# Kernel tuning notes

Hardware: AMD Instinct MI355X
Metric: run time of the kernel (lower is better)

## Reference

```python
import jax, jax.numpy as jnp
import numpy as np

TEMPERATURE = 1.0
EPS = 1e-12  # matches torch F.normalize default eps


def setup_inputs() -> dict:
    key = jax.random.key(0)
    k1, k2 = jax.random.split(key)
    B, N, D = 8, 2048, 768
    final_features = jax.random.normal(k1, (B, N, D), dtype=jnp.float32)
    mid_features = jax.random.normal(k2, (B, N, D), dtype=jnp.float32)
    return {"final_features": final_features, "mid_features": mid_features}


def reference(final_features, mid_features):
    B, N, D = final_features.shape
    dtype = final_features.dtype

    mid = mid_features.astype(jnp.float32)
    # L2-normalize along feature dim (torch F.normalize: x / max(||x||, eps))
    norm = jnp.maximum(jnp.linalg.norm(mid, axis=-1, keepdims=True), EPS)
    mid_n = mid / norm

    # [B, N, N] cosine similarity
    sim = jnp.einsum("bnd,bmd->bnm", mid_n, mid_n)
    # zero out diagonal (add_self_similarity=False): sim * (1 - eye)
    eye = jnp.eye(N, dtype=sim.dtype)
    sim = sim * (1.0 - eye)[None, :, :]

    # confidence = row-wise max of (zeroed-diagonal) similarity
    confidence = jnp.max(sim, axis=-1)  # [B, N]

    # softmax over scaled similarities (diagonal entries are exactly 0, kept in softmax)
    weights = jax.nn.softmax(sim / TEMPERATURE, axis=-1)  # [B, N, N]

    refined = jnp.einsum("bnm,bmd->bnd", weights, final_features.astype(jnp.float32))

    cw = confidence[..., None].astype(dtype)  # [B, N, 1]
    calibrated = cw * refined.astype(dtype) + (1.0 - cw) * final_features
    return calibrated
```

## Files before the change

### kernel.cpp

```cpp
#include <hip/hip_runtime.h>
#include <hip/hip_bf16.h>

static constexpr int BB = 8;
static constexpr int NN = 2048;
static constexpr int DD = 768;

typedef __attribute__((ext_vector_type(8))) __bf16 bf16x8;
typedef __attribute__((ext_vector_type(4))) float f32x4;

__device__ __forceinline__ void gload_lds16(const __hip_bfloat16* g, __hip_bfloat16* l) {
  __builtin_amdgcn_global_load_lds(
      (const __attribute__((address_space(1))) void*)g,
      (__attribute__((address_space(3))) void*)l,
      16, 0, 0);
}

__global__ void normalize_kernel(const float* __restrict__ mid, __hip_bfloat16* __restrict__ Qn,
                                 float* __restrict__ lsum, float* __restrict__ conf) {
  const int wave = threadIdx.x >> 6;
  const int lane = threadIdx.x & 63;
  const size_t row = (size_t)blockIdx.x * 4 + wave;
  if (lane == 0) { lsum[row] = 0.f; conf[row] = 0.f; }
  const float* src = mid + row * DD;

  float4 v[3];
  float ss = 0.f;
#pragma unroll
  for (int j = 0; j < 3; ++j) {
    v[j] = *(const float4*)(src + j * 256 + lane * 4);
    ss += v[j].x * v[j].x + v[j].y * v[j].y + v[j].z * v[j].z + v[j].w * v[j].w;
  }
#pragma unroll
  for (int o = 32; o; o >>= 1) ss += __shfl_xor(ss, o, 64);
  const float inv = 1.0f / fmaxf(sqrtf(ss), 1e-12f);

  __hip_bfloat16* dst = Qn + row * DD;
#pragma unroll
  for (int j = 0; j < 3; ++j) {
    union { ushort4 u; __hip_bfloat16 h[4]; } pk;
    pk.h[0] = __float2bfloat16(v[j].x * inv);
    pk.h[1] = __float2bfloat16(v[j].y * inv);
    pk.h[2] = __float2bfloat16(v[j].z * inv);
    pk.h[3] = __float2bfloat16(v[j].w * inv);
    *(ushort4*)(dst + j * 256 + lane * 4) = pk.u;
  }
}

__global__ void transpose_kernel(const float* __restrict__ F, __hip_bfloat16* __restrict__ Vt) {
  __shared__ __hip_bfloat16 tile[32][33];
  const int b = blockIdx.z;
  const int n0 = blockIdx.y * 32;
  const int d0 = blockIdx.x * 32;
  const int tx = threadIdx.x, ty = threadIdx.y;
#pragma unroll
  for (int i = 0; i < 4; ++i) {
    const int n = n0 + ty + i * 8;
    tile[ty + i * 8][tx] = __float2bfloat16(F[((size_t)b * NN + n) * DD + d0 + tx]);
  }
  __syncthreads();
#pragma unroll
  for (int i = 0; i < 4; ++i) {
    const int d = d0 + ty + i * 8;
    Vt[((size_t)b * DD + d) * NN + n0 + tx] = tile[tx][ty + i * 8];
  }
}

static constexpr int PTL = 136;
__global__ __launch_bounds__(256) void gemm_qk_kernel(
    const __hip_bfloat16* __restrict__ Qn,
    __hip_bfloat16* __restrict__ P,
    float* __restrict__ lsum,
    unsigned* __restrict__ conf) {
  __shared__ __hip_bfloat16 smem[4 * 128 * 64];

  const int d = blockIdx.x;
  const int b = d & 7;
  int rem = d >> 3;
  int ti = 0;
  while (rem >= 16 - ti) { rem -= 16 - ti; ++ti; }
  const int tj = ti + rem;
  const int rowBase = ti * 128;
  const int colBase = tj * 128;
  const bool offdiag = (ti != tj);

  const int t = threadIdx.x;
  const int lane = t & 63;
  const int wave = t >> 6;
  const int wRow = wave >> 1;
  const int wCol = wave & 1;
  const int quad = lane >> 4;
  const int l16 = lane & 15;

  const __hip_bfloat16* Abase = Qn + ((size_t)b * NN + rowBase) * DD;
  const __hip_bfloat16* Bbase = Qn + ((size_t)b * NN + colBase) * DD;

  int srow[4], scol[4], sc8[4];
#pragma unroll
  for (int i = 0; i < 4; ++i) {
    const int c = i * 256 + t;
    srow[i] = c >> 3;
    const int col8 = (c & 7) ^ ((c >> 3) & 7);
    scol[i] = col8 * 8;
    sc8[i] = c * 8;
  }

  f32x4 acc[4][4];
#pragma unroll
  for (int i = 0; i < 4; ++i)
#pragma unroll
    for (int j = 0; j < 4; ++j) acc[i][j] = (f32x4){0.f, 0.f, 0.f, 0.f};

  {
    __hip_bfloat16* As = smem;
    __hip_bfloat16* Bs = smem + 128 * 64;
#pragma unroll
    for (int i = 0; i < 4; ++i) {
      gload_lds16(Abase + (size_t)srow[i] * DD + scol[i], As + sc8[i]);
      gload_lds16(Bbase + (size_t)srow[i] * DD + scol[i], Bs + sc8[i]);
    }
  }

  constexpr int NK = DD / 64;
  for (int kk = 0; kk < NK; ++kk) {
    const int cur = kk & 1;
    __syncthreads();
    if (kk + 1 < NK) {
      __hip_bfloat16* As = smem + (1 - cur) * 2 * 128 * 64;
      __hip_bfloat16* Bs = As + 128 * 64;
      const int k0 = (kk + 1) * 64;
#pragma unroll
      for (int i = 0; i < 4; ++i) {
        gload_lds16(Abase + (size_t)srow[i] * DD + (k0 + scol[i]), As + sc8[i]);
        gload_lds16(Bbase + (size_t)srow[i] * DD + (k0 + scol[i]), Bs + sc8[i]);
      }
    }
    const __hip_bfloat16* As = smem + cur * 2 * 128 * 64;
    const __hip_bfloat16* Bs = As + 128 * 64;
#pragma unroll
    for (int ks = 0; ks < 2; ++ks) {
      bf16x8 af[4], bfr[4];
#pragma unroll
      for (int i = 0; i < 4; ++i) {
        const int rA = wRow * 64 + i * 16 + l16;
        const int rB = wCol * 64 + i * 16 + l16;
        const int pA = (ks * 4 + quad) ^ (rA & 7);
        const int pB = (ks * 4 + quad) ^ (rB & 7);
        af[i]  = *(const bf16x8*)(As + rA * 64 + pA * 8);
        bfr[i] = *(const bf16x8*)(Bs + rB * 64 + pB * 8);
      }
#pragma unroll
      for (int mi = 0; mi < 4; ++mi)
#pragma unroll
        for (int ni = 0; ni < 4; ++ni)
          acc[mi][ni] = __builtin_amdgcn_mfma_f32_16x16x32_bf16(af[mi], bfr[ni], acc[mi][ni], 0, 0, 0);
    }
  }

  __syncthreads();
  __hip_bfloat16* Pt = smem;

  float csum[4] = {0.f, 0.f, 0.f, 0.f};
  float cmax[4] = {0.f, 0.f, 0.f, 0.f};

#pragma unroll
  for (int mi = 0; mi < 4; ++mi) {
#pragma unroll
    for (int r = 0; r < 4; ++r) {
      const int rowL = wRow * 64 + mi * 16 + quad * 4 + r;
      const int row_g = rowBase + rowL;
      float ps = 0.f;
      float mx = 0.f;
#pragma unroll
      for (int ni = 0; ni < 4; ++ni) {
        const int colL = wCol * 64 + ni * 16 + l16;
        const int col_g = colBase + colL;
        float s = acc[mi][ni][r];
        if (row_g == col_g) s = 0.f;
        const float p = __expf(s);
        mx = fmaxf(mx, s);
        ps += p;
        csum[ni] += p;
        cmax[ni] = fmaxf(cmax[ni], s);
        Pt[rowL * PTL + colL] = __float2bfloat16(p);
      }
#pragma unroll
      for (int o = 1; o < 16; o <<= 1) {
        ps += __shfl_xor(ps, o, 64);
        mx = fmaxf(mx, __shfl_xor(mx, o, 64));
      }
      if (l16 == 0) {
        atomicAdd(lsum + (size_t)b * NN + row_g, ps);
        atomicMax(conf + (size_t)b * NN + row_g, __float_as_uint(mx));
      }
    }
  }

  if (offdiag) {
#pragma unroll
    for (int ni = 0; ni < 4; ++ni) {
      float cs = csum[ni];
      float cm = cmax[ni];
      cs += __shfl_xor(cs, 16, 64); cm = fmaxf(cm, __shfl_xor(cm, 16, 64));
      cs += __shfl_xor(cs, 32, 64); cm = fmaxf(cm, __shfl_xor(cm, 32, 64));
      if (quad == 0) {
        const int col_g = colBase + wCol * 64 + ni * 16 + l16;
        atomicAdd(lsum + (size_t)b * NN + col_g, cs);
        atomicMax(conf + (size_t)b * NN + col_g, __float_as_uint(cm));
      }
    }
  }

  __syncthreads();
  {
    const size_t pBase = ((size_t)b * NN + rowBase) * (size_t)NN + colBase;
#pragma unroll
    for (int i = 0; i < 8; ++i) {
      const int c = i * 256 + t;
      const int row = c >> 4;
      const int ck = c & 15;
      *(uint4*)(P + pBase + (size_t)row * NN + ck * 8) = *(const uint4*)(Pt + row * PTL + ck * 8);
    }
  }

  if (offdiag) {
    __syncthreads();
#pragma unroll
    for (int mi = 0; mi < 4; ++mi) {
#pragma unroll
      for (int ni = 0; ni < 4; ++ni) {
        const int colL = wCol * 64 + ni * 16 + l16;
        const int rbase = wRow * 64 + mi * 16 + quad * 4;
        union { ushort4 u; __hip_bfloat16 h[4]; } pk;
#pragma unroll
        for (int r = 0; r < 4; ++r) pk.h[r] = __float2bfloat16(__expf(acc[mi][ni][r]));
        *(ushort4*)(Pt + colL * PTL + rbase) = pk.u;
      }
    }
    __syncthreads();
    const size_t pBase = ((size_t)b * NN + colBase) * (size_t)NN + rowBase;
#pragma unroll
    for (int i = 0; i < 8; ++i) {
      const int c = i * 256 + t;
      const int row = c >> 4;
      const int ck = c & 15;
      *(uint4*)(P + pBase + (size_t)row * NN + ck * 8) = *(const uint4*)(Pt + row * PTL + ck * 8);
    }
  }
}

__global__ __launch_bounds__(256) void gemm_pv_kernel(
    const __hip_bfloat16* __restrict__ P,
    const __hip_bfloat16* __restrict__ Vt,
    const float* __restrict__ lsum,
    const float* __restrict__ conf,
    const float* __restrict__ F,
    float* __restrict__ Out) {
  __shared__ __hip_bfloat16 smem[4 * 128 * 64];

  const int d = blockIdx.x;
  const int work = (d & 7) * 96 + (d >> 3);
  const int colBase = (work % 6) * 128;
  const int rowBase = ((work / 6) & 15) * 128;
  const int b = work / 96;

  const int t = threadIdx.x;
  const int lane = t & 63;
  const int wave = t >> 6;
  const int wRow = wave >> 1;
  const int wCol = wave & 1;
  const int quad = lane >> 4;
  const int l16 = lane & 15;

  const __hip_bfloat16* Abase = P + (size_t)b * NN * NN + (size_t)rowBase * NN;
  const __hip_bfloat16* Bbase = Vt + (size_t)b * DD * NN + (size_t)colBase * NN;

  int srow[4], scol[4], sc8[4];
#pragma unroll
  for (int i = 0; i < 4; ++i) {
    const int c = i * 256 + t;
    srow[i] = c >> 3;
    const int col8 = (c & 7) ^ ((c >> 3) & 7);
    scol[i] = col8 * 8;
    sc8[i] = c * 8;
  }

  f32x4 acc[4][4];
#pragma unroll
  for (int i = 0; i < 4; ++i)
#pragma unroll
    for (int j = 0; j < 4; ++j) acc[i][j] = (f32x4){0.f, 0.f, 0.f, 0.f};

  {
    __hip_bfloat16* As = smem;
    __hip_bfloat16* Bs = smem + 128 * 64;
#pragma unroll
    for (int i = 0; i < 4; ++i) {
      gload_lds16(Abase + (size_t)srow[i] * NN + scol[i], As + sc8[i]);
      gload_lds16(Bbase + (size_t)srow[i] * NN + scol[i], Bs + sc8[i]);
    }
  }

  constexpr int NK = NN / 64;
  for (int kk = 0; kk < NK; ++kk) {
    const int cur = kk & 1;
    __syncthreads();
    if (kk + 1 < NK) {
      __hip_bfloat16* As = smem + (1 - cur) * 2 * 128 * 64;
      __hip_bfloat16* Bs = As + 128 * 64;
      const int k0 = (kk + 1) * 64;
#pragma unroll
      for (int i = 0; i < 4; ++i) {
        gload_lds16(Abase + (size_t)srow[i] * NN + (k0 + scol[i]), As + sc8[i]);
        gload_lds16(Bbase + (size_t)srow[i] * NN + (k0 + scol[i]), Bs + sc8[i]);
      }
    }
    const __hip_bfloat16* As = smem + cur * 2 * 128 * 64;
    const __hip_bfloat16* Bs = As + 128 * 64;
#pragma unroll
    for (int ks = 0; ks < 2; ++ks) {
      bf16x8 af[4], bfr[4];
#pragma unroll
      for (int i = 0; i < 4; ++i) {
        const int rA = wRow * 64 + i * 16 + l16;
        const int rB = wCol * 64 + i * 16 + l16;
        const int pA = (ks * 4 + quad) ^ (rA & 7);
        const int pB = (ks * 4 + quad) ^ (rB & 7);
        af[i]  = *(const bf16x8*)(As + rA * 64 + pA * 8);
        bfr[i] = *(const bf16x8*)(Bs + rB * 64 + pB * 8);
      }
#pragma unroll
      for (int mi = 0; mi < 4; ++mi)
#pragma unroll
        for (int ni = 0; ni < 4; ++ni)
          acc[mi][ni] = __builtin_amdgcn_mfma_f32_16x16x32_bf16(af[mi], bfr[ni], acc[mi][ni], 0, 0, 0);
    }
  }

#pragma unroll
  for (int mi = 0; mi < 4; ++mi) {
#pragma unroll
    for (int r = 0; r < 4; ++r) {
      const int row_g = rowBase + wRow * 64 + mi * 16 + quad * 4 + r;
      const float li = lsum[(size_t)b * NN + row_g];
      const float cw = conf[(size_t)b * NN + row_g];
      const float inv = 1.0f / li;
      const float* frow = F + ((size_t)b * NN + row_g) * DD;
      float* orow = Out + ((size_t)b * NN + row_g) * DD;
#pragma unroll
      for (int ni = 0; ni < 4; ++ni) {
        const int col_g = colBase + wCol * 64 + ni * 16 + l16;
        const float o = acc[mi][ni][r] * inv;
        orow[col_g] = cw * o + (1.f - cw) * frow[col_g];
      }
    }
  }
}

extern "C" void kernel_launch(void* const* d_in, const int* in_sizes, int n_in,
                              void* d_out, int out_size, void* d_ws, size_t ws_size,
                              hipStream_t stream) {
  const float* F = (const float*)d_in[0];
  const float* M = (const float*)d_in[1];
  float* Out = (float*)d_out;

  char* ws = (char*)d_ws;
  __hip_bfloat16* Qn = (__hip_bfloat16*)(ws);
  __hip_bfloat16* Vt = (__hip_bfloat16*)(ws + 25165824);
  __hip_bfloat16* P  = (__hip_bfloat16*)(ws + 50331648);
  float* lsum        = (float*)(ws + 117440512);
  float* conf        = (float*)(ws + 117506048);

  normalize_kernel<<<(BB * NN) / 4, 256, 0, stream>>>(M, Qn, lsum, conf);
  transpose_kernel<<<dim3(DD / 32, NN / 32, BB), dim3(32, 8), 0, stream>>>(F, Vt);
  gemm_qk_kernel<<<8 * 136, 256, 0, stream>>>(Qn, P, lsum, (unsigned*)conf);
  gemm_pv_kernel<<<768, 256, 0, stream>>>(P, Vt, lsum, conf, F, Out);
}
```

Baseline: 291.2 us.

## Merge prep kernels and write transposed P tile in same epilogue pass

```diff
diff --git a/kernel.cpp b/kernel.cpp
--- a/kernel.cpp
+++ b/kernel.cpp
@@ -15,57 +15,64 @@
       16, 0, 0);
 }
 
-__global__ void normalize_kernel(const float* __restrict__ mid, __hip_bfloat16* __restrict__ Qn,
-                                 float* __restrict__ lsum, float* __restrict__ conf) {
-  const int wave = threadIdx.x >> 6;
-  const int lane = threadIdx.x & 63;
-  const size_t row = (size_t)blockIdx.x * 4 + wave;
-  if (lane == 0) { lsum[row] = 0.f; conf[row] = 0.f; }
-  const float* src = mid + row * DD;
-
-  float4 v[3];
-  float ss = 0.f;
-#pragma unroll
-  for (int j = 0; j < 3; ++j) {
-    v[j] = *(const float4*)(src + j * 256 + lane * 4);
-    ss += v[j].x * v[j].x + v[j].y * v[j].y + v[j].z * v[j].z + v[j].w * v[j].w;
-  }
-#pragma unroll
-  for (int o = 32; o; o >>= 1) ss += __shfl_xor(ss, o, 64);
-  const float inv = 1.0f / fmaxf(sqrtf(ss), 1e-12f);
-
-  __hip_bfloat16* dst = Qn + row * DD;
-#pragma unroll
-  for (int j = 0; j < 3; ++j) {
-    union { ushort4 u; __hip_bfloat16 h[4]; } pk;
-    pk.h[0] = __float2bfloat16(v[j].x * inv);
-    pk.h[1] = __float2bfloat16(v[j].y * inv);
-    pk.h[2] = __float2bfloat16(v[j].z * inv);
-    pk.h[3] = __float2bfloat16(v[j].w * inv);
-    *(ushort4*)(dst + j * 256 + lane * 4) = pk.u;
-  }
-}
-
-__global__ void transpose_kernel(const float* __restrict__ F, __hip_bfloat16* __restrict__ Vt) {
+static constexpr int NORM_BLOCKS = (BB * NN) / 4;
+static constexpr int TRANS_BLOCKS = (DD / 32) * (NN / 32) * BB;
+__global__ void prep_kernel(const float* __restrict__ mid, __hip_bfloat16* __restrict__ Qn,
+                            float* __restrict__ lsum, float* __restrict__ conf,
+                            const float* __restrict__ F, __hip_bfloat16* __restrict__ Vt) {
   __shared__ __hip_bfloat16 tile[32][33];
-  const int b = blockIdx.z;
-  const int n0 = blockIdx.y * 32;
-  const int d0 = blockIdx.x * 32;
-  const int tx = threadIdx.x, ty = threadIdx.y;
-#pragma unroll
-  for (int i = 0; i < 4; ++i) {
-    const int n = n0 + ty + i * 8;
-    tile[ty + i * 8][tx] = __float2bfloat16(F[((size_t)b * NN + n) * DD + d0 + tx]);
-  }
-  __syncthreads();
-#pragma unroll
-  for (int i = 0; i < 4; ++i) {
-    const int d = d0 + ty + i * 8;
-    Vt[((size_t)b * DD + d) * NN + n0 + tx] = tile[tx][ty + i * 8];
-  }
-}
-
-static constexpr int PTL = 136;
+  const int t = threadIdx.x;
+  if (blockIdx.x < NORM_BLOCKS) {
+    const int wave = t >> 6;
+    const int lane = t & 63;
+    const size_t row = (size_t)blockIdx.x * 4 + wave;
+    if (lane == 0) { lsum[row] = 0.f; conf[row] = 0.f; }
+    const float* src = mid + row * DD;
+
+    float4 v[3];
+    float ss = 0.f;
+#pragma unroll
+    for (int j = 0; j < 3; ++j) {
+      v[j] = *(const float4*)(src + j * 256 + lane * 4);
+      ss += v[j].x * v[j].x + v[j].y * v[j].y + v[j].z * v[j].z + v[j].w * v[j].w;
+    }
+#pragma unroll
+    for (int o = 32; o; o >>= 1) ss += __shfl_xor(ss, o, 64);
+    const float inv = 1.0f / fmaxf(sqrtf(ss), 1e-12f);
+
+    __hip_bfloat16* dst = Qn + row * DD;
+#pragma unroll
+    for (int j = 0; j < 3; ++j) {
+      union { ushort4 u; __hip_bfloat16 h[4]; } pk;
+      pk.h[0] = __float2bfloat16(v[j].x * inv);
+      pk.h[1] = __float2bfloat16(v[j].y * inv);
+      pk.h[2] = __float2bfloat16(v[j].z * inv);
+      pk.h[3] = __float2bfloat16(v[j].w * inv);
+      *(ushort4*)(dst + j * 256 + lane * 4) = pk.u;
+    }
+  } else {
+    const int bid = blockIdx.x - NORM_BLOCKS;
+    const int bx = bid % 24;
+    const int rest = bid / 24;
+    const int by = rest & 63;
+    const int b = rest >> 6;
+    const int n0 = by * 32;
+    const int d0 = bx * 32;
+    const int tx = t & 31, ty = t >> 5;
+#pragma unroll
+    for (int i = 0; i < 4; ++i) {
+      const int n = n0 + ty + i * 8;
+      tile[ty + i * 8][tx] = __float2bfloat16(F[((size_t)b * NN + n) * DD + d0 + tx]);
+    }
+    __syncthreads();
+#pragma unroll
+    for (int i = 0; i < 4; ++i) {
+      const int d = d0 + ty + i * 8;
+      Vt[((size_t)b * DD + d) * NN + n0 + tx] = tile[tx][ty + i * 8];
+    }
+  }
+}
+
 __global__ __launch_bounds__(256) void gemm_qk_kernel(
     const __hip_bfloat16* __restrict__ Qn,
     __hip_bfloat16* __restrict__ P,
@@ -158,37 +165,48 @@
 
   __syncthreads();
   __hip_bfloat16* Pt = smem;
+  __hip_bfloat16* Mt = smem + 128 * 128;
 
   float csum[4] = {0.f, 0.f, 0.f, 0.f};
   float cmax[4] = {0.f, 0.f, 0.f, 0.f};
 
 #pragma unroll
   for (int mi = 0; mi < 4; ++mi) {
-#pragma unroll
-    for (int r = 0; r < 4; ++r) {
-      const int rowL = wRow * 64 + mi * 16 + quad * 4 + r;
-      const int row_g = rowBase + rowL;
-      float ps = 0.f;
-      float mx = 0.f;
-#pragma unroll
-      for (int ni = 0; ni < 4; ++ni) {
-        const int colL = wCol * 64 + ni * 16 + l16;
-        const int col_g = colBase + colL;
+    const int rbase = wRow * 64 + mi * 16 + quad * 4;
+    float rs[4] = {0.f, 0.f, 0.f, 0.f};
+    float rm[4] = {0.f, 0.f, 0.f, 0.f};
+#pragma unroll
+    for (int ni = 0; ni < 4; ++ni) {
+      const int colL = wCol * 64 + ni * 16 + l16;
+      const int col_g = colBase + colL;
+      union { ushort4 u; __hip_bfloat16 h[4]; } pk;
+#pragma unroll
+      for (int r = 0; r < 4; ++r) {
+        const int rowL = rbase + r;
         float s = acc[mi][ni][r];
-        if (row_g == col_g) s = 0.f;
+        if (rowBase + rowL == col_g) s = 0.f;
         const float p = __expf(s);
-        mx = fmaxf(mx, s);
-        ps += p;
+        rm[r] = fmaxf(rm[r], s);
+        rs[r] += p;
         csum[ni] += p;
         cmax[ni] = fmaxf(cmax[ni], s);
-        Pt[rowL * PTL + colL] = __float2bfloat16(p);
-      }
+        pk.h[r] = __float2bfloat16(p);
+        Pt[rowL * 128 + (((colL >> 3) ^ (rowL & 7)) << 3) + (colL & 7)] = pk.h[r];
+      }
+      if (offdiag) {
+        *(ushort4*)(Mt + colL * 128 + (((rbase >> 3) ^ (colL & 7)) << 3) + (rbase & 7)) = pk.u;
+      }
+    }
+#pragma unroll
+    for (int r = 0; r < 4; ++r) {
+      float ps = rs[r], mx = rm[r];
 #pragma unroll
       for (int o = 1; o < 16; o <<= 1) {
         ps += __shfl_xor(ps, o, 64);
         mx = fmaxf(mx, __shfl_xor(mx, o, 64));
       }
       if (l16 == 0) {
+        const int row_g = rowBase + rbase + r;
         atomicAdd(lsum + (size_t)b * NN + row_g, ps);
         atomicMax(conf + (size_t)b * NN + row_g, __float_as_uint(mx));
       }
@@ -218,32 +236,19 @@
       const int c = i * 256 + t;
       const int row = c >> 4;
       const int ck = c & 15;
-      *(uint4*)(P + pBase + (size_t)row * NN + ck * 8) = *(const uint4*)(Pt + row * PTL + ck * 8);
-    }
-  }
-
+      *(uint4*)(P + pBase + (size_t)row * NN + ck * 8) =
+          *(const uint4*)(Pt + row * 128 + ((ck ^ (row & 7)) << 3));
+    }
+  }
   if (offdiag) {
-    __syncthreads();
-#pragma unroll
-    for (int mi = 0; mi < 4; ++mi) {
-#pragma unroll
-      for (int ni = 0; ni < 4; ++ni) {
-        const int colL = wCol * 64 + ni * 16 + l16;
-        const int rbase = wRow * 64 + mi * 16 + quad * 4;
-        union { ushort4 u; __hip_bfloat16 h[4]; } pk;
-#pragma unroll
-        for (int r = 0; r < 4; ++r) pk.h[r] = __float2bfloat16(__expf(acc[mi][ni][r]));
-        *(ushort4*)(Pt + colL * PTL + rbase) = pk.u;
-      }
-    }
-    __syncthreads();
     const size_t pBase = ((size_t)b * NN + colBase) * (size_t)NN + rowBase;
 #pragma unroll
     for (int i = 0; i < 8; ++i) {
       const int c = i * 256 + t;
       const int row = c >> 4;
       const int ck = c & 15;
-      *(uint4*)(P + pBase + (size_t)row * NN + ck * 8) = *(const uint4*)(Pt + row * PTL + ck * 8);
+      *(uint4*)(P + pBase + (size_t)row * NN + ck * 8) =
+          *(const uint4*)(Mt + row * 128 + ((ck ^ (row & 7)) << 3));
     }
   }
 }
@@ -370,8 +375,7 @@
   float* lsum        = (float*)(ws + 117440512);
   float* conf        = (float*)(ws + 117506048);
 
-  normalize_kernel<<<(BB * NN) / 4, 256, 0, stream>>>(M, Qn, lsum, conf);
-  transpose_kernel<<<dim3(DD / 32, NN / 32, BB), dim3(32, 8), 0, stream>>>(F, Vt);
+  prep_kernel<<<NORM_BLOCKS + TRANS_BLOCKS, 256, 0, stream>>>(M, Qn, lsum, conf, F, Vt);
   gemm_qk_kernel<<<8 * 136, 256, 0, stream>>>(Qn, P, lsum, (unsigned*)conf);
   gemm_pv_kernel<<<768, 256, 0, stream>>>(P, Vt, lsum, conf, F, Out);
 }
```

Result: faster. 268.4 us (-7.8%).
